# Kernel tuning notes

Measured on AMD Instinct MI355X. Metric: run time of the kernel, lower is better.

Reference implementation:

```python
import jax, jax.numpy as jnp
import numpy as np

RADIUS = 2.0      # ball radius (meters)
NSAMPLE = 32      # max neighbors per ball
B = 4             # number of scenes (batch)
NPB = 4096        # points per scene (equal counts assumed)
C = 20            # number of semantic classes
CUBE = 20.0       # points live in a [0,20]^3 m cube


def setup_inputs() -> dict:
    key = jax.random.key(0)
    k1, k2, k3 = jax.random.split(key, 3)
    xyz = jax.random.uniform(k1, (B * NPB, 3), jnp.float32) * CUBE
    pred = jax.random.normal(k2, (B * NPB, C), jnp.float32)
    labels = jax.random.randint(k3, (B * NPB,), 0, C)
    tgt = jax.nn.one_hot(labels, C, dtype=jnp.float32)
    cnt = jnp.full((B,), NPB, dtype=jnp.int32)
    # module asserts new_xyz == xyz and equal batch counts
    return {"xyz": xyz, "xyz_batch_cnt": cnt, "pred": pred, "tgt": tgt,
            "new_xyz": xyz, "new_xyz_batch_cnt": cnt}


def _ball_query(xyz_b, new_xyz_b, radius, nsample):
    """xyz_b, new_xyz_b: (B, n, 3). Returns local idx (B, n, nsample).
    Replicates pointnet2 stack ball_query: first `nsample` points (in index
    order) with squared distance < radius^2; unfilled slots repeat the first
    found index. Indices are local to each batch segment."""
    n = xyz_b.shape[1]
    d2 = jnp.sum((new_xyz_b[:, :, None, :] - xyz_b[:, None, :, :]) ** 2, axis=-1)  # (B,n,n)
    mask = d2 < radius * radius
    # score = point index if inside ball else sentinel n; smallest scores = first hits
    score = jnp.where(mask, jnp.arange(n, dtype=jnp.int32), jnp.int32(n))
    neg_vals, _ = jax.lax.top_k(-score, nsample)   # largest of -score == smallest score
    idx = -neg_vals                                # (B,n,nsample), ascending index order
    first = idx[:, :, :1]                          # first found index (self is always in-ball)
    idx = jnp.where(idx == n, first, idx)          # fill empty slots with first index
    return idx


def _group(feats_b, idx_b):
    """feats_b: (B, n, C); idx_b: (B, m, nsample) local indices -> (B, m, nsample, C)."""
    b = jnp.arange(feats_b.shape[0])[:, None, None]
    return feats_b[b, idx_b]


def reference(xyz, xyz_batch_cnt, pred, tgt, new_xyz, new_xyz_batch_cnt):
    nb = xyz_batch_cnt.shape[0]
    n = xyz.shape[0] // nb                 # equal per-batch counts
    xyz_b = xyz.reshape(nb, n, 3)
    new_xyz_b = new_xyz.reshape(nb, n, 3)

    idx_b = _ball_query(xyz_b, new_xyz_b, RADIUS, NSAMPLE)   # (B,n,ns)
    m = nb * n
    idx = idx_b.reshape(m, NSAMPLE)

    # grouping_operation -> (M, C, nsample)
    grouped_pred = _group(pred.reshape(nb, n, -1), idx_b).reshape(m, NSAMPLE, -1).transpose(0, 2, 1)
    grouped_tgt = _group(tgt.reshape(nb, n, -1), idx_b).reshape(m, NSAMPLE, -1).transpose(0, 2, 1)

    # since new_xyz == xyz, every ball contains its own center -> empty_ball_mask
    # is all-False and the nonempty filtering in the torch code is the identity.
    pred_local_relation = grouped_pred - pred[:, :, None]
    tgt_local_relation = grouped_tgt - tgt[:, :, None]

    # weight (computed under no_grad in torch)
    eq = idx == idx[:, :1]
    not_eq = ~eq
    not_eq = not_eq.at[:, 0].set(True)
    a = not_eq.astype(jnp.float32)
    weight = a / jnp.sum(a, axis=-1, keepdims=True)
    return (pred_local_relation, tgt_local_relation, weight)
```

## Files before the change

### kernel.cpp

```cpp
#include <hip/hip_runtime.h>

#define NS 32
#define GX 10
#define GY 10
#define NCELL (GX * GY)
#define CAP 96
#define INV_CELL 0.5f
#define MARGIN 1e-3f

__global__ void zero_kernel(int* __restrict__ cnt, int ntot)
{
    int i = blockIdx.x * 256 + threadIdx.x;
    if (i < ntot) cnt[i] = 0;
}

__global__ __launch_bounds__(256) void bin_kernel(
    const float* __restrict__ xyz, int n, int total,
    int* __restrict__ cnt, float4* __restrict__ cellpts)
{
    int i = blockIdx.x * 256 + threadIdx.x;
    if (i >= total) return;
    int b  = i / n;
    int il = i - b * n;
    float x = xyz[3 * i + 0], y = xyz[3 * i + 1], z = xyz[3 * i + 2];
    int cx = (int)floorf(x * INV_CELL); cx = min(max(cx, 0), GX - 1);
    int cy = (int)floorf(y * INV_CELL); cy = min(max(cy, 0), GY - 1);
    int cell = b * NCELL + cx * GY + cy;
    int pos = atomicAdd(&cnt[cell], 1);
    if (pos < CAP)
        cellpts[(size_t)cell * CAP + pos] = make_float4(x, y, z, __int_as_float(il));
}

template <int C>
__global__ __launch_bounds__(256) void query_kernel(
    const float* __restrict__ new_xyz,
    const float* __restrict__ pred, const float* __restrict__ tgt,
    const int* __restrict__ cnt, const float4* __restrict__ cellpts,
    int n, int total,
    float* __restrict__ out0, float* __restrict__ out1, float* __restrict__ wout)
{
#pragma clang fp contract(off)
    __shared__ int slist[4][64];

    const int lane = threadIdx.x & 63;
    const int wv   = __builtin_amdgcn_readfirstlane(threadIdx.x >> 6);
    const int q    = blockIdx.x * 4 + wv;
    if (q >= total) return;
    const int b    = q / n;
    const int base = b * n;

    const float qx = new_xyz[q * 3 + 0];
    const float qy = new_xyz[q * 3 + 1];
    const float qz = new_xyz[q * 3 + 2];

    int cx0 = (int)floorf((qx - 2.0f - MARGIN) * INV_CELL); cx0 = max(cx0, 0);
    int cx1 = (int)floorf((qx + 2.0f + MARGIN) * INV_CELL); cx1 = min(cx1, GX - 1);
    int cy0 = (int)floorf((qy - 2.0f - MARGIN) * INV_CELL); cy0 = max(cy0, 0);
    int cy1 = (int)floorf((qy + 2.0f + MARGIN) * INV_CELL); cy1 = min(cy1, GY - 1);

    int tot = 0;
    const int bb = b * NCELL;
    for (int cx = cx0; cx <= cx1; ++cx) {
        for (int cy = cy0; cy <= cy1; ++cy) {
            const int cell = bb + cx * GY + cy;
            int cc = cnt[cell]; cc = cc < CAP ? cc : CAP;
            const float4* __restrict__ pl = cellpts + (size_t)cell * CAP;
            for (int r = 0; r < cc; r += 64) {
                const int  t   = r + lane;
                const bool act = t < cc;
                const float4 f = pl[act ? t : 0];
                float dx = qx - f.x, dy = qy - f.y, dz = qz - f.z;
                float d2 = (dx * dx + dy * dy) + dz * dz;
                const bool hit = act && (d2 < 4.0f);
                const unsigned long long m = __ballot(hit);
                const int pos = tot + __builtin_amdgcn_mbcnt_hi(
                    (unsigned)(m >> 32), __builtin_amdgcn_mbcnt_lo((unsigned)m, 0u));
                if (hit && pos < 64) slist[wv][pos] = __float_as_int(f.w);
                tot += __popcll(m);
            }
        }
    }

    int v = (lane < tot) ? slist[wv][lane] : 0x7fffffff;
    #pragma unroll
    for (int k = 2; k <= 64; k <<= 1) {
        #pragma unroll
        for (int j = k >> 1; j >= 1; j >>= 1) {
            const int  o     = __shfl_xor(v, j, 64);
            const bool up    = ((lane & k) == 0);
            const bool lower = ((lane & j) == 0);
            const int  mn = v < o ? v : o;
            const int  mx = v < o ? o : v;
            v = (lower == up) ? mn : mx;
        }
    }

    const int tc    = tot < NS ? tot : NS;
    const int firstv = __shfl(v, 0, 64);
    const int first = (tot > 0) ? firstv : (n - 1);
    const int s     = lane & 31;
    const int jl0   = __shfl(v, s, 64);
    const int jl    = (s < tc) ? jl0 : first;

    const int tcm = tc > 0 ? tc : 1;
    if (lane < NS)
        wout[(size_t)q * NS + lane] = (lane < tcm) ? 1.0f / (float)tcm : 0.0f;

    const float* __restrict__ src = (lane >> 5) ? tgt : pred;
    float* __restrict__ dst       = (lane >> 5) ? out1 : out0;
    const float4* __restrict__ nb = (const float4*)(src + (size_t)(base + jl) * C);
    const float4* __restrict__ ct = (const float4*)(src + (size_t)q * C);
    float* __restrict__ o = dst + (size_t)q * (C * NS) + s;
    #pragma unroll
    for (int c4 = 0; c4 < C / 4; ++c4) {
        const float4 a = nb[c4], bq = ct[c4];
        o[(c4 * 4 + 0) * NS] = a.x - bq.x;
        o[(c4 * 4 + 1) * NS] = a.y - bq.y;
        o[(c4 * 4 + 2) * NS] = a.z - bq.z;
        o[(c4 * 4 + 3) * NS] = a.w - bq.w;
    }
    #pragma unroll
    for (int c = (C / 4) * 4; c < C; ++c)
        o[c * NS] = src[(size_t)(base + jl) * C + c] - src[(size_t)q * C + c];
}

template <int C>
__global__ __launch_bounds__(256) void fused_brute_kernel(
    const float* __restrict__ xyz, const float* __restrict__ new_xyz,
    const float* __restrict__ pred, const float* __restrict__ tgt,
    int n, int total, float* __restrict__ out0, float* __restrict__ out1,
    float* __restrict__ wout)
{
#pragma clang fp contract(off)
    __shared__ int sidx[8][NS];

    const int lane = threadIdx.x & 63;
    const int wv   = __builtin_amdgcn_readfirstlane(threadIdx.x >> 6);
    int q0 = (blockIdx.x * 4 + wv) * 2;
    if (q0 > total - 2) q0 = total - 2;
    const int base = (q0 / n) * n;

    const float ax0 = new_xyz[q0 * 3 + 0], ay0 = new_xyz[q0 * 3 + 1], az0 = new_xyz[q0 * 3 + 2];
    const float ax1 = new_xyz[q0 * 3 + 3], ay1 = new_xyz[q0 * 3 + 4], az1 = new_xyz[q0 * 3 + 5];
    const float* __restrict__ px = xyz + (size_t)base * 3;

    int tot0 = 0, tot1 = 0, first0 = n - 1, first1 = n - 1;
    for (int it = 0; it < n; it += 64) {
        const int ja  = it + lane;
        const int jca = ja < n ? ja : n - 1;
        const float xa = px[jca * 3 + 0], ya = px[jca * 3 + 1], za = px[jca * 3 + 2];
        float dx = ax0 - xa, dy = ay0 - ya, dz = az0 - za;
        const float d0 = (dx * dx + dy * dy) + dz * dz;
        dx = ax1 - xa; dy = ay1 - ya; dz = az1 - za;
        const float d1 = (dx * dx + dy * dy) + dz * dz;
        const bool h0 = (ja < n) & (d0 < 4.0f);
        const bool h1 = (ja < n) & (d1 < 4.0f);
        const unsigned long long m0 = __ballot(h0);
        if (m0) {
            if (tot0 == 0) first0 = it + __builtin_ctzll(m0);
            const int pos = tot0 + __builtin_amdgcn_mbcnt_hi(
                (unsigned)(m0 >> 32), __builtin_amdgcn_mbcnt_lo((unsigned)m0, 0u));
            if (h0 && pos < NS) sidx[wv * 2 + 0][pos] = ja;
            tot0 += __popcll(m0);
        }
        const unsigned long long m1 = __ballot(h1);
        if (m1) {
            if (tot1 == 0) first1 = it + __builtin_ctzll(m1);
            const int pos = tot1 + __builtin_amdgcn_mbcnt_hi(
                (unsigned)(m1 >> 32), __builtin_amdgcn_mbcnt_lo((unsigned)m1, 0u));
            if (h1 && pos < NS) sidx[wv * 2 + 1][pos] = ja;
            tot1 += __popcll(m1);
        }
    }

    const int s  = lane & 31;
    const int qs = lane >> 5;
    {
        const int tt    = qs ? tot1 : tot0;
        const int first = qs ? first1 : first0;
        const int tc    = tt < NS ? tt : NS;
        if (s >= tc) sidx[wv * 2 + qs][s] = first;
        const int tcm = tc > 0 ? tc : 1;
        wout[(size_t)q0 * NS + lane] = (s < tcm) ? 1.0f / (float)tcm : 0.0f;
    }
    __syncthreads();

    const int q  = q0 + qs;
    const int jl = sidx[wv * 2 + qs][s];
    const float4* __restrict__ nb_p = (const float4*)(pred + (size_t)(base + jl) * C);
    const float4* __restrict__ nb_t = (const float4*)(tgt  + (size_t)(base + jl) * C);
    const float4* __restrict__ ct_p = (const float4*)(pred + (size_t)q * C);
    const float4* __restrict__ ct_t = (const float4*)(tgt  + (size_t)q * C);
    float* __restrict__ o0 = out0 + (size_t)q * (C * NS) + s;
    float* __restrict__ o1 = out1 + (size_t)q * (C * NS) + s;
    #pragma unroll
    for (int c4 = 0; c4 < C / 4; ++c4) {
        const float4 a = nb_p[c4], bq = ct_p[c4];
        o0[(c4 * 4 + 0) * NS] = a.x - bq.x;
        o0[(c4 * 4 + 1) * NS] = a.y - bq.y;
        o0[(c4 * 4 + 2) * NS] = a.z - bq.z;
        o0[(c4 * 4 + 3) * NS] = a.w - bq.w;
        const float4 u = nb_t[c4], vv = ct_t[c4];
        o1[(c4 * 4 + 0) * NS] = u.x - vv.x;
        o1[(c4 * 4 + 1) * NS] = u.y - vv.y;
        o1[(c4 * 4 + 2) * NS] = u.z - vv.z;
        o1[(c4 * 4 + 3) * NS] = u.w - vv.w;
    }
}

extern "C" void kernel_launch(void* const* d_in, const int* in_sizes, int n_in,
                              void* d_out, int out_size, void* d_ws, size_t ws_size,
                              hipStream_t stream)
{
    const float* xyz     = (const float*)d_in[0];
    const float* pred    = (const float*)d_in[2];
    const float* tgt     = (const float*)d_in[3];
    const float* new_xyz = (const float*)d_in[4];

    const int total = in_sizes[0] / 3;
    const int nb    = in_sizes[1];
    const int n     = total / nb;
    const int C     = in_sizes[2] / total;

    float* out = (float*)d_out;
    const size_t relsz = (size_t)total * C * NS;
    float* out0 = out;
    float* out1 = out + relsz;
    float* wout = out + 2 * relsz;

    const int ncells = nb * NCELL;
    const size_t ws_need = (size_t)ncells * CAP * sizeof(float4) + (size_t)ncells * sizeof(int);

    if (C == 20 && ws_size >= ws_need) {
        float4* cellpts = (float4*)d_ws;
        int*    cnt     = (int*)((char*)d_ws + (size_t)ncells * CAP * sizeof(float4));

        zero_kernel<<<(ncells + 255) / 256, 256, 0, stream>>>(cnt, ncells);
        bin_kernel<<<(total + 255) / 256, 256, 0, stream>>>(xyz, n, total, cnt, cellpts);
        query_kernel<20><<<(total + 3) / 4, 256, 0, stream>>>(
            new_xyz, pred, tgt, cnt, cellpts, n, total, out0, out1, wout);
    } else if (C == 20) {
        fused_brute_kernel<20><<<(total + 7) / 8, 256, 0, stream>>>(
            xyz, new_xyz, pred, tgt, n, total, out0, out1, wout);
    }
    (void)n_in; (void)out_size;
}
```

Measured before the change: 41.61 us.

## Switch to 3D uniform grid with per-wave candidate table and sorted cells

Replaces the 2D column binning with a 10x10x10 voxel grid (cap 32 per cell), adds a kernel that bitonic-sorts each cell's points by index, and makes the query wave build a flattened candidate index table in LDS via a prefix scan over the up-to-27 neighbor cells. Candidates are then streamed in full 64-lane batches, which removes the many partially filled iterations over z-columns and cuts distance tests per query. It adds a launch, a large LDS table per block that may limit occupancy, and block-wide __syncthreads (which is why out-of-range waves are clamped instead of returning). Cell overflow beyond 32 points would drop neighbors, and hits beyond 64 are truncated before the sort.

Measured after the change: 53.59 us. +28.8%, slower.

```diff
diff --git a/kernel.cpp b/kernel.cpp
--- a/kernel.cpp
+++ b/kernel.cpp
@@ -1,12 +1,12 @@
 #include <hip/hip_runtime.h>
 
 #define NS 32
-#define GX 10
-#define GY 10
-#define NCELL (GX * GY)
-#define CAP 96
+#define GD 10
+#define NC3 (GD * GD * GD)
+#define CAP 32
 #define INV_CELL 0.5f
 #define MARGIN 1e-3f
+#define CAND_MAX (64 * CAP)
 
 __global__ void zero_kernel(int* __restrict__ cnt, int ntot)
 {
@@ -23,12 +23,54 @@
     int b  = i / n;
     int il = i - b * n;
     float x = xyz[3 * i + 0], y = xyz[3 * i + 1], z = xyz[3 * i + 2];
-    int cx = (int)floorf(x * INV_CELL); cx = min(max(cx, 0), GX - 1);
-    int cy = (int)floorf(y * INV_CELL); cy = min(max(cy, 0), GY - 1);
-    int cell = b * NCELL + cx * GY + cy;
+    int cx = min(max((int)floorf(x * INV_CELL), 0), GD - 1);
+    int cy = min(max((int)floorf(y * INV_CELL), 0), GD - 1);
+    int cz = min(max((int)floorf(z * INV_CELL), 0), GD - 1);
+    int cell = ((b * GD + cx) * GD + cy) * GD + cz;
     int pos = atomicAdd(&cnt[cell], 1);
     if (pos < CAP)
         cellpts[(size_t)cell * CAP + pos] = make_float4(x, y, z, __int_as_float(il));
+}
+
+__global__ __launch_bounds__(256) void sort_cells_kernel(
+    const int* __restrict__ cnt, float4* __restrict__ cellpts, int ncells)
+{
+    const int lane = threadIdx.x & 63;
+    const int wv   = threadIdx.x >> 6;
+    const int cell = blockIdx.x * 4 + wv;
+    if (cell >= ncells) return;
+    int cc = cnt[cell];
+    cc = cc < CAP ? cc : CAP;
+    if (cc <= 1) return;
+
+    float4 f = make_float4(0.f, 0.f, 0.f, 0.f);
+    int key = 0x7fffffff;
+    if (lane < cc) {
+        f   = cellpts[(size_t)cell * CAP + lane];
+        key = __float_as_int(f.w);
+    }
+    int src = lane;
+
+    #pragma unroll
+    for (int k = 2; k <= 64; k <<= 1) {
+        #pragma unroll
+        for (int j = k >> 1; j >= 1; j >>= 1) {
+            const int  ok    = __shfl_xor(key, j, 64);
+            const int  os    = __shfl_xor(src, j, 64);
+            const bool up    = ((lane & k) == 0);
+            const bool lower = ((lane & j) == 0);
+            const bool takeMin = (lower == up);
+            const bool keep = takeMin ? (key <= ok) : (key >= ok);
+            key = keep ? key : ok;
+            src = keep ? src : os;
+        }
+    }
+    const float sx = __shfl(f.x, src, 64);
+    const float sy = __shfl(f.y, src, 64);
+    const float sz = __shfl(f.z, src, 64);
+    const float sw = __shfl(f.w, src, 64);
+    if (lane < cc)
+        cellpts[(size_t)cell * CAP + lane] = make_float4(sx, sy, sz, sw);
 }
 
 template <int C>
@@ -40,12 +82,13 @@
     float* __restrict__ out0, float* __restrict__ out1, float* __restrict__ wout)
 {
 #pragma clang fp contract(off)
+    __shared__ int stab[4][CAND_MAX];
     __shared__ int slist[4][64];
 
     const int lane = threadIdx.x & 63;
     const int wv   = __builtin_amdgcn_readfirstlane(threadIdx.x >> 6);
-    const int q    = blockIdx.x * 4 + wv;
-    if (q >= total) return;
+    int q = blockIdx.x * 4 + wv;
+    if (q >= total) q = total - 1;
     const int b    = q / n;
     const int base = b * n;
 
@@ -53,35 +96,64 @@
     const float qy = new_xyz[q * 3 + 1];
     const float qz = new_xyz[q * 3 + 2];
 
-    int cx0 = (int)floorf((qx - 2.0f - MARGIN) * INV_CELL); cx0 = max(cx0, 0);
-    int cx1 = (int)floorf((qx + 2.0f + MARGIN) * INV_CELL); cx1 = min(cx1, GX - 1);
-    int cy0 = (int)floorf((qy - 2.0f - MARGIN) * INV_CELL); cy0 = max(cy0, 0);
-    int cy1 = (int)floorf((qy + 2.0f + MARGIN) * INV_CELL); cy1 = min(cy1, GY - 1);
+    int cx0 = max((int)floorf((qx - 2.0f - MARGIN) * INV_CELL), 0);
+    int cx1 = min((int)floorf((qx + 2.0f + MARGIN) * INV_CELL), GD - 1);
+    int cy0 = max((int)floorf((qy - 2.0f - MARGIN) * INV_CELL), 0);
+    int cy1 = min((int)floorf((qy + 2.0f + MARGIN) * INV_CELL), GD - 1);
+    int cz0 = max((int)floorf((qz - 2.0f - MARGIN) * INV_CELL), 0);
+    int cz1 = min((int)floorf((qz + 2.0f + MARGIN) * INV_CELL), GD - 1);
+    const int ny = cy1 - cy0 + 1, nz = cz1 - cz0 + 1;
+    const int ncell = __builtin_amdgcn_readfirstlane((cx1 - cx0 + 1) * ny * nz);
+
+    int cc = 0, gbase = 0;
+    if (lane < ncell) {
+        int lx  = lane / (ny * nz);
+        int rem = lane - lx * (ny * nz);
+        int ly  = rem / nz;
+        int lz  = rem - ly * nz;
+        int cell = ((b * GD + (cx0 + lx)) * GD + (cy0 + ly)) * GD + (cz0 + lz);
+        int c = cnt[cell];
+        cc    = c < CAP ? c : CAP;
+        gbase = cell * CAP;
+    }
+    int run = cc;
+    #pragma unroll
+    for (int off = 1; off < 64; off <<= 1) {
+        int y = __shfl_up(run, off, 64);
+        if (lane >= off) run += y;
+    }
+    const int pref = run - cc;
+    const int T = __shfl(run, ncell - 1, 64);
+
+    for (int k = 0; k < ncell; ++k) {
+        const int cck   = __shfl(cc, k, 64);
+        const int prefk = __shfl(pref, k, 64);
+        const int gbk   = __shfl(gbase, k, 64);
+        if (lane < cck) stab[wv][prefk + lane] = gbk + lane;
+    }
+
+    __syncthreads();
 
     int tot = 0;
-    const int bb = b * NCELL;
-    for (int cx = cx0; cx <= cx1; ++cx) {
-        for (int cy = cy0; cy <= cy1; ++cy) {
-            const int cell = bb + cx * GY + cy;
-            int cc = cnt[cell]; cc = cc < CAP ? cc : CAP;
-            const float4* __restrict__ pl = cellpts + (size_t)cell * CAP;
-            for (int r = 0; r < cc; r += 64) {
-                const int  t   = r + lane;
-                const bool act = t < cc;
-                const float4 f = pl[act ? t : 0];
-                float dx = qx - f.x, dy = qy - f.y, dz = qz - f.z;
-                float d2 = (dx * dx + dy * dy) + dz * dz;
-                const bool hit = act && (d2 < 4.0f);
-                const unsigned long long m = __ballot(hit);
-                const int pos = tot + __builtin_amdgcn_mbcnt_hi(
-                    (unsigned)(m >> 32), __builtin_amdgcn_mbcnt_lo((unsigned)m, 0u));
-                if (hit && pos < 64) slist[wv][pos] = __float_as_int(f.w);
-                tot += __popcll(m);
-            }
-        }
-    }
-
-    int v = (lane < tot) ? slist[wv][lane] : 0x7fffffff;
+    for (int r = 0; r < T; r += 64) {
+        const int  t   = r + lane;
+        const bool act = t < T;
+        const int  ai  = stab[wv][act ? t : 0];
+        const float4 f = cellpts[ai];
+        float dx = qx - f.x, dy = qy - f.y, dz = qz - f.z;
+        float d2 = (dx * dx + dy * dy) + dz * dz;
+        const bool hit = act && (d2 < 4.0f);
+        const unsigned long long m = __ballot(hit);
+        const int pos = tot + __builtin_amdgcn_mbcnt_hi(
+            (unsigned)(m >> 32), __builtin_amdgcn_mbcnt_lo((unsigned)m, 0u));
+        if (hit && pos < 64) slist[wv][pos] = __float_as_int(f.w);
+        tot += __popcll(m);
+    }
+
+    __syncthreads();
+
+    const int totv = tot < 64 ? tot : 64;
+    int v = (lane < totv) ? slist[wv][lane] : 0x7fffffff;
     #pragma unroll
     for (int k = 2; k <= 64; k <<= 1) {
         #pragma unroll
@@ -95,12 +167,12 @@
         }
     }
 
-    const int tc    = tot < NS ? tot : NS;
+    const int tc     = tot < NS ? tot : NS;
     const int firstv = __shfl(v, 0, 64);
-    const int first = (tot > 0) ? firstv : (n - 1);
-    const int s     = lane & 31;
-    const int jl0   = __shfl(v, s, 64);
-    const int jl    = (s < tc) ? jl0 : first;
+    const int first  = (tot > 0) ? firstv : (n - 1);
+    const int s      = lane & 31;
+    const int jl0    = __shfl(v, s, 64);
+    const int jl     = (s < tc) ? jl0 : first;
 
     const int tcm = tc > 0 ? tc : 1;
     if (lane < NS)
@@ -228,7 +300,7 @@
     float* out1 = out + relsz;
     float* wout = out + 2 * relsz;
 
-    const int ncells = nb * NCELL;
+    const int ncells = nb * NC3;
     const size_t ws_need = (size_t)ncells * CAP * sizeof(float4) + (size_t)ncells * sizeof(int);
 
     if (C == 20 && ws_size >= ws_need) {
@@ -237,6 +309,7 @@
 
         zero_kernel<<<(ncells + 255) / 256, 256, 0, stream>>>(cnt, ncells);
         bin_kernel<<<(total + 255) / 256, 256, 0, stream>>>(xyz, n, total, cnt, cellpts);
+        sort_cells_kernel<<<(ncells + 3) / 4, 256, 0, stream>>>(cnt, cellpts, ncells);
         query_kernel<20><<<(total + 3) / 4, 256, 0, stream>>>(
             new_xyz, pred, tgt, cnt, cellpts, n, total, out0, out1, wout);
     } else if (C == 20) {
```
